# Kernel optimization log

Measured on AMD Instinct MI355X. Metric: run time of the kernel, lower is better.

Reference implementation:

```python
import jax, jax.numpy as jnp
import numpy as np

N = 50000

def gcn_conv(x, W, b, src, dst, n):
    # x: [N, Fin], W: [Fin, Fout]; PyG GCNConv: transform then sym-normalized aggregate (self-loops included in src/dst)
    h = x @ W  # [N, Fout]
    deg = jax.ops.segment_sum(jnp.ones_like(dst, dtype=h.dtype), dst, num_segments=n)
    inv_sqrt = jnp.where(deg > 0, jax.lax.rsqrt(deg), 0.0)
    norm = inv_sqrt[src] * inv_sqrt[dst]  # [E+N]
    msg = h[src] * norm[:, None]
    out = jax.ops.segment_sum(msg, dst, num_segments=n)
    return out + b


def setup_inputs() -> dict:
    key = jax.random.key(0)
    ks = jax.random.split(key, 8)
    d_in, d_h, n_exp, E = 64, 64, 16, 800000
    x = jax.random.normal(ks[0], (N, d_in), dtype=jnp.float32)
    edge_index = jax.random.randint(ks[1], (2, E), 0, N, dtype=jnp.int64)
    s = 1.0 / np.sqrt(d_in)
    W1 = jax.random.uniform(ks[2], (d_in, d_h), minval=-s, maxval=s, dtype=jnp.float32)
    b1 = jnp.zeros((d_h,), jnp.float32)
    W2 = jax.random.uniform(ks[3], (d_h, d_h), minval=-s, maxval=s, dtype=jnp.float32)
    b2 = jnp.zeros((d_h,), jnp.float32)
    Wc = jax.random.uniform(ks[4], (d_h, n_exp), minval=-s, maxval=s, dtype=jnp.float32)
    bc = jnp.zeros((n_exp,), jnp.float32)
    return {"x": x, "edge_index": edge_index, "W1": W1, "b1": b1, "W2": W2, "b2": b2, "Wc": Wc, "bc": bc}


def reference(x, edge_index, W1, b1, W2, b2, Wc, bc):
    # add self-loops once (PyG GCNConv default add_self_loops=True)
    loops = jnp.arange(N, dtype=edge_index.dtype)
    src = jnp.concatenate([edge_index[0], loops])
    dst = jnp.concatenate([edge_index[1], loops])
    h = jax.nn.relu(gcn_conv(x, W1, b1, src, dst, N))
    # dropout is identity in eval mode
    h = jax.nn.relu(gcn_conv(h, W2, b2, src, dst, N))
    return h @ Wc + bc
```

## Files before the change

### kernel.cpp

```cpp
#include <hip/hip_runtime.h>
#include <hip/hip_fp16.h>


#define FDIM 64
#define NCLS 16
#define TILE 2048
#define BSH 7
#define BSZ 128

__global__ __launch_bounds__(256) void k_histgemm(const int* __restrict__ dst, int E,
                                                  int* __restrict__ H, int nblk,
                                                  const float* __restrict__ X,
                                                  const float* __restrict__ W,
                                                  __half* __restrict__ Yh, int n) {
    __shared__ float Ws[FDIM * FDIM];
    __shared__ int h[512];
    int t = threadIdx.x, blk = blockIdx.x;
    if (blk < nblk) {
        h[t] = 0;
        h[t + 256] = 0;
        __syncthreads();
        int i0 = blk * TILE;
#pragma unroll
        for (int k = 0; k < TILE / 256; ++k) {
            int i = i0 + k * 256 + t;
            if (i < E) atomicAdd(&h[dst[i] >> BSH], 1);
        }
        __syncthreads();
        H[blk * 512 + t] = h[t];
        H[blk * 512 + t + 256] = h[t + 256];
    } else {
        for (int i = t; i < FDIM * FDIM; i += 256) Ws[i] = W[i];
        __syncthreads();
        if (blk == nblk && t < 8)
            ((uint4*)Yh)[(size_t)n * 8 + t] = make_uint4(0, 0, 0, 0);
        int idx = (blk - nblk) * 256 + t;
        int row = idx >> 2;
        int cg = (idx & 3) * 16;
        if (row >= n) return;
        const float4* xr = (const float4*)(X + (size_t)row * FDIM);
        float4 xv[16];
#pragma unroll
        for (int i = 0; i < 16; ++i) xv[i] = xr[i];
        float acc[16];
#pragma unroll
        for (int c = 0; c < 16; ++c) acc[c] = 0.f;
#pragma unroll
        for (int i = 0; i < 16; ++i) {
            float xs[4] = {xv[i].x, xv[i].y, xv[i].z, xv[i].w};
#pragma unroll
            for (int j = 0; j < 4; ++j) {
                float xk = xs[j];
                const float* wr = &Ws[(i * 4 + j) * FDIM + cg];
#pragma unroll
                for (int c = 0; c < 16; ++c) acc[c] += xk * wr[c];
            }
        }
        unsigned u[8];
#pragma unroll
        for (int i = 0; i < 8; ++i) {
            __half2 hp = __floats2half2_rn(acc[2 * i], acc[2 * i + 1]);
            u[i] = *(unsigned*)&hp;
        }
        uint4* yo = (uint4*)(Yh + (size_t)row * FDIM + cg);
        yo[0] = make_uint4(u[0], u[1], u[2], u[3]);
        yo[1] = make_uint4(u[4], u[5], u[6], u[7]);
    }
}

__global__ __launch_bounds__(512) void k_scanH(int* __restrict__ H, int nblk, int* __restrict__ btot) {
    __shared__ int s[512];
    int t = threadIdx.x, b = blockIdx.x;
    int v = (t < nblk) ? H[t * 512 + b] : 0;
    s[t] = v;
    __syncthreads();
    for (int off = 1; off < 512; off <<= 1) {
        int add = (t >= off) ? s[t - off] : 0;
        __syncthreads();
        s[t] += add;
        __syncthreads();
    }
    if (t < nblk) H[t * 512 + b] = s[t] - v;
    if (t == 511) btot[b] = s[511];
}

__global__ __launch_bounds__(512) void k_scatA(const int* __restrict__ src, const int* __restrict__ dst,
                                               int E, const int* __restrict__ H,
                                               const int* __restrict__ btot, int nb,
                                               unsigned* __restrict__ tmp) {
    __shared__ int s[512];
    __shared__ int Hb[512];
    __shared__ int c2[512];
    int t = threadIdx.x, blk = blockIdx.x;
    int v = (t < nb) ? btot[t] : 0;
    s[t] = v;
    __syncthreads();
    for (int off = 1; off < 512; off <<= 1) {
        int add = (t >= off) ? s[t - off] : 0;
        __syncthreads();
        s[t] += add;
        __syncthreads();
    }
    Hb[t] = (s[t] - v) + H[blk * 512 + t];
    c2[t] = 0;
    __syncthreads();
    int i0 = blk * TILE;
#pragma unroll
    for (int k = 0; k < TILE / 512; ++k) {
        int i = i0 + k * 512 + t;
        if (i < E) {
            int sv = src[i], d = dst[i];
            int b = d >> BSH;
            unsigned rec = ((unsigned)(d & (BSZ - 1)) << 16) | (unsigned)sv;
            int pos = Hb[b] + atomicAdd(&c2[b], 1);
            tmp[pos] = rec;
        }
    }
}

#define COLCAP 6144
__global__ __launch_bounds__(512) void k_binB(const unsigned* __restrict__ tmp,
                                              const int* __restrict__ btot, int nb,
                                              int n, int E, int* __restrict__ row_ptr,
                                              float* __restrict__ inv,
                                              unsigned short* __restrict__ col,
                                              __half* __restrict__ P1) {
    __shared__ int dcnt[BSZ], cur[BSZ], s[512];
    __shared__ float ivS[BSZ];
    __shared__ unsigned short colbuf[COLCAP];
    __shared__ int baseS;
    int t = threadIdx.x, b = blockIdx.x;
    int v = (t < nb) ? btot[t] : 0;
    s[t] = v;
    __syncthreads();
    for (int off = 1; off < 512; off <<= 1) {
        int add = (t >= off) ? s[t - off] : 0;
        __syncthreads();
        s[t] += add;
        __syncthreads();
    }
    if (t == b) baseS = s[t] - v;
    if (t < BSZ) dcnt[t] = 0;
    __syncthreads();
    int base = baseS;
    int pbase = ((base + 7) & ~7) + b * 2048;
    int cntE = btot[b];
    int node0 = b << BSH;
    int nn = min(BSZ, n - node0);
    for (int i = t; i < cntE; i += 512) atomicAdd(&dcnt[tmp[base + i] >> 16], 1);
    __syncthreads();
    int deg = 0, pdeg = 0;
    if (t < BSZ) {
        deg = dcnt[t];
        pdeg = (deg + 15) & ~15;
        s[t] = pdeg;
    }
    __syncthreads();
    for (int off = 1; off < BSZ; off <<= 1) {
        int add = 0;
        if (t < BSZ && t >= off) add = s[t - off];
        __syncthreads();
        if (t < BSZ) s[t] += add;
        __syncthreads();
    }
    int pexcl = (t < BSZ) ? (s[t] - pdeg) : 0;
    int ptot = s[BSZ - 1];
    if (t < BSZ) {
        float ivv = rsqrtf((float)(deg + 1));
        ivS[t] = ivv;
        if (t < nn) {
            row_ptr[node0 + t] = (pbase + pexcl) | ((pdeg >> 4) << 22);
            inv[node0 + t] = ivv;
        }
    }
    if (b == 0 && t == 0) inv[n] = 0.f;
    if (t < BSZ) cur[t] = pexcl;
    __syncthreads();
    for (int i = t; i < cntE; i += 512) {
        unsigned r = tmp[base + i];
        int pos = atomicAdd(&cur[r >> 16], 1);
        unsigned short vv = (unsigned short)(r & 0xFFFFu);
        if (pos < COLCAP) colbuf[pos] = vv;
        else col[pbase + pos] = vv;
    }
    if (t < nn) {
        int p1 = pexcl + pdeg;
        for (int p = pexcl + deg; p < p1; ++p) {
            if (p < COLCAP) colbuf[p] = (unsigned short)n;
            else col[pbase + p] = (unsigned short)n;
        }
    }
    __syncthreads();
    int lim = min(ptot, COLCAP);
    for (int i = t; i < lim; i += 512) col[pbase + i] = colbuf[i];
    {
        int fl = t & 7;
        for (int r = t >> 3; r < nn; r += 64) {
            float ivr = ivS[r];
            uint4* pr = (uint4*)P1 + (size_t)(node0 + r) * 8 + fl;
            uint4 q = *pr;
            float2 f0 = __half22float2(*(__half2*)&q.x);
            float2 f1 = __half22float2(*(__half2*)&q.y);
            float2 f2 = __half22float2(*(__half2*)&q.z);
            float2 f3 = __half22float2(*(__half2*)&q.w);
            __half2 h0 = __floats2half2_rn(f0.x * ivr, f0.y * ivr);
            __half2 h1 = __floats2half2_rn(f1.x * ivr, f1.y * ivr);
            __half2 h2 = __floats2half2_rn(f2.x * ivr, f2.y * ivr);
            __half2 h3 = __floats2half2_rn(f3.x * ivr, f3.y * ivr);
            *pr = make_uint4(*(unsigned*)&h0, *(unsigned*)&h1,
                             *(unsigned*)&h2, *(unsigned*)&h3);
        }
    }
}

__device__ __forceinline__ void unpack8(const uint4& q, float* f) {
    float2 f0 = __half22float2(*(const __half2*)&q.x);
    float2 f1 = __half22float2(*(const __half2*)&q.y);
    float2 f2 = __half22float2(*(const __half2*)&q.z);
    float2 f3 = __half22float2(*(const __half2*)&q.w);
    f[0] = f0.x; f[1] = f0.y; f[2] = f1.x; f[3] = f1.y;
    f[4] = f2.x; f[5] = f2.y; f[6] = f3.x; f[7] = f3.y;
}
__device__ __forceinline__ void decode8(const uint4& cv, int* c) {
    c[0] = cv.x & 0xFFFF; c[1] = cv.x >> 16;
    c[2] = cv.y & 0xFFFF; c[3] = cv.y >> 16;
    c[4] = cv.z & 0xFFFF; c[5] = cv.z >> 16;
    c[6] = cv.w & 0xFFFF; c[7] = cv.w >> 16;
}

__global__ __launch_bounds__(256) void k_aggF1(const __half* __restrict__ Ph, const float* __restrict__ inv,
                                               const int* __restrict__ row_ptr,
                                               const unsigned short* __restrict__ col,
                                               const float* __restrict__ bias,
                                               const float* __restrict__ W2,
                                               __half* __restrict__ P2, int n) {
    __shared__ float W2s[FDIM * FDIM];
    __shared__ float rbuf[32][FDIM + 1];
    int t0 = threadIdx.x;
    for (int i = t0; i < FDIM * FDIM; i += 256) W2s[i] = W2[i];
    if (blockIdx.x == 0 && t0 < 8)
        ((uint4*)P2)[(size_t)n * 8 + t0] = make_uint4(0, 0, 0, 0);
    int lane = t0 & 63;
    int sub = lane >> 3;
    int fl = lane & 7;
    int wid = t0 >> 6;
    int nl = wid * 8 + sub;
    int node = blockIdx.x * 32 + nl;
    bool alive = node < n;
    int nodeC = alive ? node : (n - 1);
    float iv = inv[nodeC];
    const uint4* Pq = (const uint4*)Ph;
    uint4 selfq = Pq[(size_t)nodeC * 8 + fl];
    float a[8], f[8];
    unpack8(selfq, a);
    int v = row_ptr[nodeC];
    int s = v & 0x3FFFFF;
    int e = alive ? s + ((v >> 22) << 4) : s;
    for (int j = s; j < e; j += 16) {
        uint4 cv0 = *(const uint4*)(col + j);
        uint4 cv1 = *(const uint4*)(col + j + 8);
        int c[16];
        decode8(cv0, c);
        decode8(cv1, c + 8);
        uint4 q[16];
#pragma unroll
        for (int k = 0; k < 16; ++k) q[k] = Pq[(size_t)c[k] * 8 + fl];
#pragma unroll
        for (int k = 0; k < 16; ++k) {
            unpack8(q[k], f);
#pragma unroll
            for (int i = 0; i < 8; ++i) a[i] += f[i];
        }
    }
    float4 bb0 = ((const float4*)bias)[fl * 2];
    float4 bb1 = ((const float4*)bias)[fl * 2 + 1];
    float bbv[8] = {bb0.x, bb0.y, bb0.z, bb0.w, bb1.x, bb1.y, bb1.z, bb1.w};
#pragma unroll
    for (int i = 0; i < 8; ++i)
        rbuf[nl][fl * 8 + i] = fmaxf(fmaf(iv, a[i], bbv[i]), 0.f);
    __syncthreads();
    int nl2 = t0 >> 3;
    int cg = t0 & 7;
    int node2 = blockIdx.x * 32 + nl2;
    const float* rr = rbuf[nl2];
    float o[8];
#pragma unroll
    for (int i = 0; i < 8; ++i) o[i] = 0.f;
#pragma unroll
    for (int i = 0; i < FDIM; ++i) {
        float xk = rr[i];
        const float* wv = &W2s[i * FDIM + cg * 8];
#pragma unroll
        for (int c = 0; c < 8; ++c) o[c] = fmaf(xk, wv[c], o[c]);
    }
    if (node2 < n) {
        float iv2 = inv[node2];
        unsigned u[4];
#pragma unroll
        for (int i = 0; i < 4; ++i) {
            __half2 hp = __floats2half2_rn(o[2 * i] * iv2, o[2 * i + 1] * iv2);
            u[i] = *(unsigned*)&hp;
        }
        ((uint4*)P2)[(size_t)node2 * 8 + cg] = make_uint4(u[0], u[1], u[2], u[3]);
    }
}

__global__ __launch_bounds__(256) void k_aggF2(const __half* __restrict__ Ph, const float* __restrict__ inv,
                                               const int* __restrict__ row_ptr,
                                               const unsigned short* __restrict__ col,
                                               const float* __restrict__ bias,
                                               const float* __restrict__ Wc, const float* __restrict__ bc,
                                               float* __restrict__ out, int n) {
    __shared__ float WcT[NCLS * FDIM];
    int t0 = threadIdx.x;
    for (int i = t0; i < FDIM * NCLS; i += 256) {
        int c = i & 15, ff = i >> 4;
        WcT[c * FDIM + ff] = Wc[i];
    }
    __syncthreads();
    int lane = t0 & 63;
    int sub = lane >> 3;
    int fl = lane & 7;
    int wid = t0 >> 6;
    int node = blockIdx.x * 32 + wid * 8 + sub;
    bool alive = node < n;
    int nodeC = alive ? node : (n - 1);
    float iv = inv[nodeC];
    const uint4* Pq = (const uint4*)Ph;
    uint4 selfq = Pq[(size_t)nodeC * 8 + fl];
    float a[8], f[8];
    unpack8(selfq, a);
    int v = row_ptr[nodeC];
    int s = v & 0x3FFFFF;
    int e = alive ? s + ((v >> 22) << 4) : s;
    for (int j = s; j < e; j += 16) {
        uint4 cv0 = *(const uint4*)(col + j);
        uint4 cv1 = *(const uint4*)(col + j + 8);
        int c[16];
        decode8(cv0, c);
        decode8(cv1, c + 8);
        uint4 q[16];
#pragma unroll
        for (int k = 0; k < 16; ++k) q[k] = Pq[(size_t)c[k] * 8 + fl];
#pragma unroll
        for (int k = 0; k < 16; ++k) {
            unpack8(q[k], f);
#pragma unroll
            for (int i = 0; i < 8; ++i) a[i] += f[i];
        }
    }
    float4 bb0 = ((const float4*)bias)[fl * 2];
    float4 bb1 = ((const float4*)bias)[fl * 2 + 1];
    float bbv[8] = {bb0.x, bb0.y, bb0.z, bb0.w, bb1.x, bb1.y, bb1.z, bb1.w};
    float r[8];
#pragma unroll
    for (int i = 0; i < 8; ++i) r[i] = fmaxf(fmaf(iv, a[i], bbv[i]), 0.f);
    float part[NCLS];
#pragma unroll
    for (int c = 0; c < NCLS; ++c) {
        float4 wv0 = ((const float4*)(WcT + c * FDIM))[fl * 2];
        float4 wv1 = ((const float4*)(WcT + c * FDIM))[fl * 2 + 1];
        part[c] = r[0] * wv0.x;
        part[c] = fmaf(r[1], wv0.y, part[c]);
        part[c] = fmaf(r[2], wv0.z, part[c]);
        part[c] = fmaf(r[3], wv0.w, part[c]);
        part[c] = fmaf(r[4], wv1.x, part[c]);
        part[c] = fmaf(r[5], wv1.y, part[c]);
        part[c] = fmaf(r[6], wv1.z, part[c]);
        part[c] = fmaf(r[7], wv1.w, part[c]);
    }
#pragma unroll
    for (int m = 1; m < 8; m <<= 1) {
#pragma unroll
        for (int c = 0; c < NCLS; ++c) part[c] += __shfl_xor(part[c], m, 64);
    }
    if (alive && fl < 4) {
        float4 bb2 = ((const float4*)bc)[fl];
        float4 o = make_float4(part[fl * 4 + 0] + bb2.x, part[fl * 4 + 1] + bb2.y,
                               part[fl * 4 + 2] + bb2.z, part[fl * 4 + 3] + bb2.w);
        ((float4*)out)[(size_t)node * 4 + fl] = o;
    }
}

static inline size_t align256(size_t x) { return (x + 255) & ~(size_t)255; }

extern "C" void kernel_launch(void* const* d_in, const int* in_sizes, int n_in,
                              void* d_out, int out_size, void* d_ws, size_t ws_size,
                              hipStream_t stream) {
    const float* x  = (const float*)d_in[0];
    const int*   ei = (const int*)d_in[1];
    const float* W1 = (const float*)d_in[2];
    const float* b1 = (const float*)d_in[3];
    const float* W2 = (const float*)d_in[4];
    const float* b2 = (const float*)d_in[5];
    const float* Wc = (const float*)d_in[6];
    const float* bc = (const float*)d_in[7];
    float* out = (float*)d_out;

    const int n = in_sizes[0] / FDIM;
    const int E = in_sizes[1] / 2;
    const int* src = ei;
    const int* dst = ei + E;

    const int nb = (n + BSZ - 1) >> BSH;
    const int nblk = (E + TILE - 1) / TILE;

    char* w = (char*)d_ws;
    size_t off = 0;
    int* H = (int*)(w + off);        off = align256(off + (size_t)nblk * 512 * 4);
    int* btot = (int*)(w + off);     off = align256(off + 512 * 4);
    int* row_ptr = (int*)(w + off);  off = align256(off + (size_t)(n + 1) * 4);
    float* inv = (float*)(w + off);  off = align256(off + (size_t)(n + 1) * 4);
    unsigned* tmp = (unsigned*)(w + off);             off = align256(off + (size_t)E * 4);
    unsigned short* col = (unsigned short*)(w + off); off = align256(off + ((size_t)E + (size_t)nb * 2048 + 128) * 2);
    __half* P1 = (__half*)(w + off); off = align256(off + (size_t)(n + 1) * FDIM * 2);
    __half* P2 = (__half*)(w + off); off = align256(off + (size_t)(n + 1) * FDIM * 2);
    (void)ws_size;

    const int nbG = (n * 4 + 255) / 256;
    const int nbA = (n + 31) / 32;

    k_histgemm<<<nblk + nbG, 256, 0, stream>>>(dst, E, H, nblk, x, W1, P1, n);
    k_scanH<<<nb, 512, 0, stream>>>(H, nblk, btot);
    k_scatA<<<nblk, 512, 0, stream>>>(src, dst, E, H, btot, nb, tmp);
    k_binB<<<nb, 512, 0, stream>>>(tmp, btot, nb, n, E, row_ptr, inv, col, P1);

    k_aggF1<<<nbA, 256, 0, stream>>>(P1, inv, row_ptr, col, b1, W2, P2, n);
    k_aggF2<<<nbA, 256, 0, stream>>>(P2, inv, row_ptr, col, b2, Wc, bc, out, n);
}
```

Before: 151.7 us.

## Split feature tables into two half-width planes and aggregate per half

Stores the transformed node features as two separate 32-column fp16 tables and runs the neighbor gather/accumulate twice, once per half. Each pass touches a smaller table, which is meant to raise cache hit rates for the random neighbor gathers. In exchange, the column index list is re-read and decoded twice, and each gather moves narrower 8-byte chunks, which raises the number of memory requests.

New measurement: 164.3 us. 8.3% more time.

```diff
diff --git a/kernel.cpp b/kernel.cpp
--- a/kernel.cpp
+++ b/kernel.cpp
@@ -12,7 +12,8 @@
                                                   int* __restrict__ H, int nblk,
                                                   const float* __restrict__ X,
                                                   const float* __restrict__ W,
-                                                  __half* __restrict__ Yh, int n) {
+                                                  __half* __restrict__ P1a,
+                                                  __half* __restrict__ P1b, int n) {
     __shared__ float Ws[FDIM * FDIM];
     __shared__ int h[512];
     int t = threadIdx.x, blk = blockIdx.x;
@@ -32,8 +33,11 @@
     } else {
         for (int i = t; i < FDIM * FDIM; i += 256) Ws[i] = W[i];
         __syncthreads();
-        if (blk == nblk && t < 8)
-            ((uint4*)Yh)[(size_t)n * 8 + t] = make_uint4(0, 0, 0, 0);
+        if (blk == nblk && t < 8) {
+            uint4 z = make_uint4(0, 0, 0, 0);
+            if (t < 4) ((uint4*)(P1a + (size_t)n * 32))[t] = z;
+            else       ((uint4*)(P1b + (size_t)n * 32))[t - 4] = z;
+        }
         int idx = (blk - nblk) * 256 + t;
         int row = idx >> 2;
         int cg = (idx & 3) * 16;
@@ -62,7 +66,8 @@
             __half2 hp = __floats2half2_rn(acc[2 * i], acc[2 * i + 1]);
             u[i] = *(unsigned*)&hp;
         }
-        uint4* yo = (uint4*)(Yh + (size_t)row * FDIM + cg);
+        __half* tab = (cg < 32) ? P1a : P1b;
+        uint4* yo = (uint4*)(tab + (size_t)row * 32 + (cg & 31));
         yo[0] = make_uint4(u[0], u[1], u[2], u[3]);
         yo[1] = make_uint4(u[4], u[5], u[6], u[7]);
     }
@@ -124,7 +129,8 @@
                                               int n, int E, int* __restrict__ row_ptr,
                                               float* __restrict__ inv,
                                               unsigned short* __restrict__ col,
-                                              __half* __restrict__ P1) {
+                                              __half* __restrict__ P1a,
+                                              __half* __restrict__ P1b) {
     __shared__ int dcnt[BSZ], cur[BSZ], s[512];
     __shared__ float ivS[BSZ];
     __shared__ unsigned short colbuf[COLCAP];
@@ -197,7 +203,9 @@
         int fl = t & 7;
         for (int r = t >> 3; r < nn; r += 64) {
             float ivr = ivS[r];
-            uint4* pr = (uint4*)P1 + (size_t)(node0 + r) * 8 + fl;
+            uint4* pr;
+            if (fl < 4) pr = (uint4*)(P1a + (size_t)(node0 + r) * 32) + fl;
+            else        pr = (uint4*)(P1b + (size_t)(node0 + r) * 32) + (fl - 4);
             uint4 q = *pr;
             float2 f0 = __half22float2(*(__half2*)&q.x);
             float2 f1 = __half22float2(*(__half2*)&q.y);
@@ -213,13 +221,10 @@
     }
 }
 
-__device__ __forceinline__ void unpack8(const uint4& q, float* f) {
+__device__ __forceinline__ void unpack4(const uint2& q, float* f) {
     float2 f0 = __half22float2(*(const __half2*)&q.x);
     float2 f1 = __half22float2(*(const __half2*)&q.y);
-    float2 f2 = __half22float2(*(const __half2*)&q.z);
-    float2 f3 = __half22float2(*(const __half2*)&q.w);
     f[0] = f0.x; f[1] = f0.y; f[2] = f1.x; f[3] = f1.y;
-    f[4] = f2.x; f[5] = f2.y; f[6] = f3.x; f[7] = f3.y;
 }
 __device__ __forceinline__ void decode8(const uint4& cv, int* c) {
     c[0] = cv.x & 0xFFFF; c[1] = cv.x >> 16;
@@ -228,18 +233,22 @@
     c[6] = cv.w & 0xFFFF; c[7] = cv.w >> 16;
 }
 
-__global__ __launch_bounds__(256) void k_aggF1(const __half* __restrict__ Ph, const float* __restrict__ inv,
+__global__ __launch_bounds__(256) void k_aggF1(const __half* __restrict__ P1a, const __half* __restrict__ P1b,
+                                               const float* __restrict__ inv,
                                                const int* __restrict__ row_ptr,
                                                const unsigned short* __restrict__ col,
                                                const float* __restrict__ bias,
                                                const float* __restrict__ W2,
-                                               __half* __restrict__ P2, int n) {
+                                               __half* __restrict__ P2a, __half* __restrict__ P2b, int n) {
     __shared__ float W2s[FDIM * FDIM];
     __shared__ float rbuf[32][FDIM + 1];
     int t0 = threadIdx.x;
     for (int i = t0; i < FDIM * FDIM; i += 256) W2s[i] = W2[i];
-    if (blockIdx.x == 0 && t0 < 8)
-        ((uint4*)P2)[(size_t)n * 8 + t0] = make_uint4(0, 0, 0, 0);
+    if (blockIdx.x == 0 && t0 < 8) {
+        uint4 z = make_uint4(0, 0, 0, 0);
+        if (t0 < 4) ((uint4*)(P2a + (size_t)n * 32))[t0] = z;
+        else        ((uint4*)(P2b + (size_t)n * 32))[t0 - 4] = z;
+    }
     int lane = t0 & 63;
     int sub = lane >> 3;
     int fl = lane & 7;
@@ -249,35 +258,38 @@
     bool alive = node < n;
     int nodeC = alive ? node : (n - 1);
     float iv = inv[nodeC];
-    const uint4* Pq = (const uint4*)Ph;
-    uint4 selfq = Pq[(size_t)nodeC * 8 + fl];
-    float a[8], f[8];
-    unpack8(selfq, a);
     int v = row_ptr[nodeC];
     int s = v & 0x3FFFFF;
     int e = alive ? s + ((v >> 22) << 4) : s;
-    for (int j = s; j < e; j += 16) {
-        uint4 cv0 = *(const uint4*)(col + j);
-        uint4 cv1 = *(const uint4*)(col + j + 8);
-        int c[16];
-        decode8(cv0, c);
-        decode8(cv1, c + 8);
-        uint4 q[16];
-#pragma unroll
-        for (int k = 0; k < 16; ++k) q[k] = Pq[(size_t)c[k] * 8 + fl];
-#pragma unroll
-        for (int k = 0; k < 16; ++k) {
-            unpack8(q[k], f);
-#pragma unroll
-            for (int i = 0; i < 8; ++i) a[i] += f[i];
-        }
-    }
-    float4 bb0 = ((const float4*)bias)[fl * 2];
-    float4 bb1 = ((const float4*)bias)[fl * 2 + 1];
-    float bbv[8] = {bb0.x, bb0.y, bb0.z, bb0.w, bb1.x, bb1.y, bb1.z, bb1.w};
-#pragma unroll
-    for (int i = 0; i < 8; ++i)
-        rbuf[nl][fl * 8 + i] = fmaxf(fmaf(iv, a[i], bbv[i]), 0.f);
+#pragma unroll
+    for (int hh = 0; hh < 2; ++hh) {
+        const uint2* Pq2 = (const uint2*)(hh ? P1b : P1a);
+        uint2 selfq = Pq2[(size_t)nodeC * 8 + fl];
+        float a4[4], f4[4];
+        unpack4(selfq, a4);
+        for (int j = s; j < e; j += 16) {
+            uint4 cv0 = *(const uint4*)(col + j);
+            uint4 cv1 = *(const uint4*)(col + j + 8);
+            int c[16];
+            decode8(cv0, c);
+            decode8(cv1, c + 8);
+            uint2 q[16];
+#pragma unroll
+            for (int k = 0; k < 16; ++k) q[k] = Pq2[(size_t)c[k] * 8 + fl];
+#pragma unroll
+            for (int k = 0; k < 16; ++k) {
+                unpack4(q[k], f4);
+#pragma unroll
+                for (int i = 0; i < 4; ++i) a4[i] += f4[i];
+            }
+        }
+        int fb = hh * 32 + fl * 4;
+        float4 bb = ((const float4*)bias)[fb >> 2];
+        rbuf[nl][fb + 0] = fmaxf(fmaf(iv, a4[0], bb.x), 0.f);
+        rbuf[nl][fb + 1] = fmaxf(fmaf(iv, a4[1], bb.y), 0.f);
+        rbuf[nl][fb + 2] = fmaxf(fmaf(iv, a4[2], bb.z), 0.f);
+        rbuf[nl][fb + 3] = fmaxf(fmaf(iv, a4[3], bb.w), 0.f);
+    }
     __syncthreads();
     int nl2 = t0 >> 3;
     int cg = t0 & 7;
@@ -301,11 +313,14 @@
             __half2 hp = __floats2half2_rn(o[2 * i] * iv2, o[2 * i + 1] * iv2);
             u[i] = *(unsigned*)&hp;
         }
-        ((uint4*)P2)[(size_t)node2 * 8 + cg] = make_uint4(u[0], u[1], u[2], u[3]);
-    }
-}
-
-__global__ __launch_bounds__(256) void k_aggF2(const __half* __restrict__ Ph, const float* __restrict__ inv,
+        uint4 val = make_uint4(u[0], u[1], u[2], u[3]);
+        if (cg < 4) ((uint4*)(P2a + (size_t)node2 * 32))[cg] = val;
+        else        ((uint4*)(P2b + (size_t)node2 * 32))[cg - 4] = val;
+    }
+}
+
+__global__ __launch_bounds__(256) void k_aggF2(const __half* __restrict__ P2a, const __half* __restrict__ P2b,
+                                               const float* __restrict__ inv,
                                                const int* __restrict__ row_ptr,
                                                const unsigned short* __restrict__ col,
                                                const float* __restrict__ bias,
@@ -326,48 +341,48 @@
     bool alive = node < n;
     int nodeC = alive ? node : (n - 1);
     float iv = inv[nodeC];
-    const uint4* Pq = (const uint4*)Ph;
-    uint4 selfq = Pq[(size_t)nodeC * 8 + fl];
-    float a[8], f[8];
-    unpack8(selfq, a);
     int v = row_ptr[nodeC];
     int s = v & 0x3FFFFF;
     int e = alive ? s + ((v >> 22) << 4) : s;
-    for (int j = s; j < e; j += 16) {
-        uint4 cv0 = *(const uint4*)(col + j);
-        uint4 cv1 = *(const uint4*)(col + j + 8);
-        int c[16];
-        decode8(cv0, c);
-        decode8(cv1, c + 8);
-        uint4 q[16];
-#pragma unroll
-        for (int k = 0; k < 16; ++k) q[k] = Pq[(size_t)c[k] * 8 + fl];
-#pragma unroll
-        for (int k = 0; k < 16; ++k) {
-            unpack8(q[k], f);
-#pragma unroll
-            for (int i = 0; i < 8; ++i) a[i] += f[i];
-        }
-    }
-    float4 bb0 = ((const float4*)bias)[fl * 2];
-    float4 bb1 = ((const float4*)bias)[fl * 2 + 1];
-    float bbv[8] = {bb0.x, bb0.y, bb0.z, bb0.w, bb1.x, bb1.y, bb1.z, bb1.w};
-    float r[8];
-#pragma unroll
-    for (int i = 0; i < 8; ++i) r[i] = fmaxf(fmaf(iv, a[i], bbv[i]), 0.f);
     float part[NCLS];
 #pragma unroll
-    for (int c = 0; c < NCLS; ++c) {
-        float4 wv0 = ((const float4*)(WcT + c * FDIM))[fl * 2];
-        float4 wv1 = ((const float4*)(WcT + c * FDIM))[fl * 2 + 1];
-        part[c] = r[0] * wv0.x;
-        part[c] = fmaf(r[1], wv0.y, part[c]);
-        part[c] = fmaf(r[2], wv0.z, part[c]);
-        part[c] = fmaf(r[3], wv0.w, part[c]);
-        part[c] = fmaf(r[4], wv1.x, part[c]);
-        part[c] = fmaf(r[5], wv1.y, part[c]);
-        part[c] = fmaf(r[6], wv1.z, part[c]);
-        part[c] = fmaf(r[7], wv1.w, part[c]);
+    for (int c = 0; c < NCLS; ++c) part[c] = 0.f;
+#pragma unroll
+    for (int hh = 0; hh < 2; ++hh) {
+        const uint2* Pq2 = (const uint2*)(hh ? P2b : P2a);
+        uint2 selfq = Pq2[(size_t)nodeC * 8 + fl];
+        float a4[4], f4[4];
+        unpack4(selfq, a4);
+        for (int j = s; j < e; j += 16) {
+            uint4 cv0 = *(const uint4*)(col + j);
+            uint4 cv1 = *(const uint4*)(col + j + 8);
+            int c[16];
+            decode8(cv0, c);
+            decode8(cv1, c + 8);
+            uint2 q[16];
+#pragma unroll
+            for (int k = 0; k < 16; ++k) q[k] = Pq2[(size_t)c[k] * 8 + fl];
+#pragma unroll
+            for (int k = 0; k < 16; ++k) {
+                unpack4(q[k], f4);
+#pragma unroll
+                for (int i = 0; i < 4; ++i) a4[i] += f4[i];
+            }
+        }
+        int fb = hh * 32 + fl * 4;
+        float4 bb = ((const float4*)bias)[fb >> 2];
+        float r0 = fmaxf(fmaf(iv, a4[0], bb.x), 0.f);
+        float r1 = fmaxf(fmaf(iv, a4[1], bb.y), 0.f);
+        float r2 = fmaxf(fmaf(iv, a4[2], bb.z), 0.f);
+        float r3 = fmaxf(fmaf(iv, a4[3], bb.w), 0.f);
+#pragma unroll
+        for (int c = 0; c < NCLS; ++c) {
+            float4 wv = *(const float4*)(WcT + c * FDIM + fb);
+            part[c] = fmaf(r0, wv.x, part[c]);
+            part[c] = fmaf(r1, wv.y, part[c]);
+            part[c] = fmaf(r2, wv.z, part[c]);
+            part[c] = fmaf(r3, wv.w, part[c]);
+        }
     }
 #pragma unroll
     for (int m = 1; m < 8; m <<= 1) {
@@ -413,18 +428,20 @@
     float* inv = (float*)(w + off);  off = align256(off + (size_t)(n + 1) * 4);
     unsigned* tmp = (unsigned*)(w + off);             off = align256(off + (size_t)E * 4);
     unsigned short* col = (unsigned short*)(w + off); off = align256(off + ((size_t)E + (size_t)nb * 2048 + 128) * 2);
-    __half* P1 = (__half*)(w + off); off = align256(off + (size_t)(n + 1) * FDIM * 2);
-    __half* P2 = (__half*)(w + off); off = align256(off + (size_t)(n + 1) * FDIM * 2);
+    __half* P1a = (__half*)(w + off); off = align256(off + (size_t)(n + 1) * 32 * 2);
+    __half* P1b = (__half*)(w + off); off = align256(off + (size_t)(n + 1) * 32 * 2);
+    __half* P2a = (__half*)(w + off); off = align256(off + (size_t)(n + 1) * 32 * 2);
+    __half* P2b = (__half*)(w + off); off = align256(off + (size_t)(n + 1) * 32 * 2);
     (void)ws_size;
 
     const int nbG = (n * 4 + 255) / 256;
     const int nbA = (n + 31) / 32;
 
-    k_histgemm<<<nblk + nbG, 256, 0, stream>>>(dst, E, H, nblk, x, W1, P1, n);
+    k_histgemm<<<nblk + nbG, 256, 0, stream>>>(dst, E, H, nblk, x, W1, P1a, P1b, n);
     k_scanH<<<nb, 512, 0, stream>>>(H, nblk, btot);
     k_scatA<<<nblk, 512, 0, stream>>>(src, dst, E, H, btot, nb, tmp);
-    k_binB<<<nb, 512, 0, stream>>>(tmp, btot, nb, n, E, row_ptr, inv, col, P1);
-
-    k_aggF1<<<nbA, 256, 0, stream>>>(P1, inv, row_ptr, col, b1, W2, P2, n);
-    k_aggF2<<<nbA, 256, 0, stream>>>(P2, inv, row_ptr, col, b2, Wc, bc, out, n);
-}
+    k_binB<<<nb, 512, 0, stream>>>(tmp, btot, nb, n, E, row_ptr, inv, col, P1a, P1b);
+
+    k_aggF1<<<nbA, 256, 0, stream>>>(P1a, P1b, inv, row_ptr, col, b1, W2, P2a, P2b, n);
+    k_aggF2<<<nbA, 256, 0, stream>>>(P2a, P2b, inv, row_ptr, col, b2, Wc, bc, out, n);
+}
```
